# Kernel tuning notes

Hardware: AMD Instinct MI355X
Metric: run time of the kernel (lower is better)

Reference implementation:

```python
import jax, jax.numpy as jnp
import numpy as np

NUM_HEADS = 4
NUM_GROUPS = 32
EPS = 1e-5

def setup_inputs() -> dict:
    key = jax.random.key(0)
    ks = jax.random.split(key, 3)
    B, C, H, W = 16, 512, 32, 32
    x = jax.random.normal(ks[0], (B, C, H, W), dtype=jnp.float32)
    gn_w = jnp.ones((C,), jnp.float32)
    gn_b = jnp.zeros((C,), jnp.float32)
    qkv_w = jax.random.normal(ks[1], (3 * C, C), dtype=jnp.float32) * (C ** -0.5)
    qkv_b = jnp.zeros((3 * C,), jnp.float32)
    proj_w = jax.random.normal(ks[2], (C, C), dtype=jnp.float32) * (C ** -0.5)
    proj_b = jnp.zeros((C,), jnp.float32)
    return {"x": x, "gn_w": gn_w, "gn_b": gn_b, "qkv_w": qkv_w,
            "qkv_b": qkv_b, "proj_w": proj_w, "proj_b": proj_b}

def group_norm(x, w, b):
    B, C, H, W = x.shape
    xg = x.reshape(B, NUM_GROUPS, C // NUM_GROUPS, H, W)
    mean = xg.mean(axis=(2, 3, 4), keepdims=True)
    var = xg.var(axis=(2, 3, 4), keepdims=True)
    xg = (xg - mean) * jax.lax.rsqrt(var + EPS)
    x = xg.reshape(B, C, H, W)
    return x * w[None, :, None, None] + b[None, :, None, None]

def reference(x, gn_w, gn_b, qkv_w, qkv_b, proj_w, proj_b):
    B, C, H, W = x.shape
    hd = C // NUM_HEADS
    h = group_norm(x, gn_w, gn_b)
    # 1x1 conv == channel matmul
    qkv = jnp.einsum('oc,bchw->bohw', qkv_w, h) + qkv_b[None, :, None, None]
    q, k, v = jnp.split(qkv, 3, axis=1)
    N = H * W
    q = q.reshape(B, NUM_HEADS, hd, N)
    k = k.reshape(B, NUM_HEADS, hd, N)
    v = v.reshape(B, NUM_HEADS, hd, N)
    scale = hd ** -0.5
    attn = jnp.einsum('bhcn,bhcm->bhnm', q, k) * scale
    attn = jax.nn.softmax(attn, axis=-1)
    o = jnp.einsum('bhnm,bhcm->bhcn', attn, v).reshape(B, C, H, W)
    o = jnp.einsum('oc,bchw->bohw', proj_w, o) + proj_b[None, :, None, None]
    return x + o
```

## Files before the change

kernel.cpp:

```cpp
#include <hip/hip_runtime.h>

typedef __attribute__((ext_vector_type(4))) float f32x4;
typedef __attribute__((ext_vector_type(8))) short s16x8;

#define MFMA16(a, b, c) __builtin_amdgcn_mfma_f32_16x16x32_bf16((a), (b), (c), 0, 0, 0)

__device__ __forceinline__ unsigned short f2bf(float f) {
    union { float f; unsigned u; } v; v.f = f;
    unsigned u = v.u + 0x7FFFu + ((v.u >> 16) & 1u);
    return (unsigned short)(u >> 16);
}

__device__ __forceinline__ unsigned cvtpk(float lo, float hi) {
    unsigned r;
    asm("v_cvt_pk_bf16_f32 %0, %1, %2" : "=v"(r) : "v"(lo), "v"(hi));
    return r;
}

__device__ __forceinline__ float exp2f_fast(float x) {
    float r;
    asm("v_exp_f32 %0, %1" : "=v"(r) : "v"(x));
    return r;
}

__device__ __forceinline__ void gll16(const unsigned short* g, unsigned short* l) {
    __builtin_amdgcn_global_load_lds((const __attribute__((address_space(1))) void*)g,
                                     (__attribute__((address_space(3))) void*)l, 16, 0, 0);
}

__global__ __launch_bounds__(256) void k_wconv(const float* __restrict__ qkv_w,
                                               const float* __restrict__ proj_w,
                                               unsigned short* __restrict__ wout) {
    int i = blockIdx.x * 256 + threadIdx.x;
    const int NQ = 3 * 512 * 512;
    float v = (i < NQ) ? qkv_w[i] : proj_w[i - NQ];
    wout[i] = f2bf(v);
}

__global__ __launch_bounds__(256) void k_gnstats(const float* __restrict__ x,
                                                 float* __restrict__ stats) {
    int bg = blockIdx.x;
    const float4* p = (const float4*)(x + (size_t)bg * 16384);
    float s = 0.f, ss = 0.f;
    for (int i = threadIdx.x; i < 4096; i += 256) {
        float4 v = p[i];
        s += v.x + v.y + v.z + v.w;
        ss += v.x * v.x + v.y * v.y + v.z * v.z + v.w * v.w;
    }
    for (int w = 1; w < 64; w <<= 1) { s += __shfl_xor(s, w); ss += __shfl_xor(ss, w); }
    __shared__ float rs[4], rss[4];
    int wid = threadIdx.x >> 6;
    if ((threadIdx.x & 63) == 0) { rs[wid] = s; rss[wid] = ss; }
    __syncthreads();
    if (threadIdx.x == 0) {
        float S = rs[0] + rs[1] + rs[2] + rs[3];
        float SS = rss[0] + rss[1] + rss[2] + rss[3];
        float mean = S * (1.f / 16384.f);
        float var = SS * (1.f / 16384.f) - mean * mean;
        stats[bg * 2] = mean;
        stats[bg * 2 + 1] = rsqrtf(var + 1e-5f);
    }
}

__global__ __launch_bounds__(256) void k_gnapply(const float* __restrict__ x,
                                                 const float* __restrict__ gnw,
                                                 const float* __restrict__ gnb,
                                                 const float* __restrict__ stats,
                                                 unsigned short* __restrict__ h_t) {
    int b = blockIdx.x >> 5, nb = blockIdx.x & 31;
    int n0 = nb * 32;
    __shared__ unsigned short lds[32][520];
    int t = threadIdx.x;
    int f4 = t & 7, c0 = t >> 3;
    for (int c = c0; c < 512; c += 32) {
        int g = c >> 4;
        float mean = stats[(b * 32 + g) * 2], rstd = stats[(b * 32 + g) * 2 + 1];
        float sc = gnw[c] * rstd;
        float sh = gnb[c] - mean * sc;
        float4 v = *(const float4*)(x + ((size_t)(b * 512 + c)) * 1024 + n0 + f4 * 4);
        lds[f4 * 4 + 0][c] = f2bf(v.x * sc + sh);
        lds[f4 * 4 + 1][c] = f2bf(v.y * sc + sh);
        lds[f4 * 4 + 2][c] = f2bf(v.z * sc + sh);
        lds[f4 * 4 + 3][c] = f2bf(v.w * sc + sh);
    }
    __syncthreads();
    int ch = t & 63;
    for (int nl = t >> 6; nl < 32; nl += 4) {
        *(uint4*)(h_t + ((size_t)(b * 1024 + n0 + nl)) * 512 + ch * 8) =
            *(const uint4*)(&lds[nl][ch * 8]);
    }
}

__global__ __launch_bounds__(256) void k_gemm(const unsigned short* __restrict__ A,
                                              const unsigned short* __restrict__ Bt,
                                              const float* __restrict__ bias, int mode,
                                              unsigned short* __restrict__ Qo,
                                              unsigned short* __restrict__ Ko,
                                              unsigned short* __restrict__ Vo,
                                              const float* __restrict__ xres,
                                              float* __restrict__ out) {
    const int Kd = 512;
    int id = blockIdx.x;
    int xcd = id & 7, j = id >> 3;
    int nt = xcd + 8 * (j & 15);
    int mt = j >> 4;
    int t = threadIdx.x, wid = t >> 6, lane = t & 63;
    int lm = lane & 15, q4 = lane >> 4;
    int wm = wid >> 1, wn = wid & 1;
    __shared__ unsigned short ldsA[2][4096];
    __shared__ unsigned short ldsB[2][4096];
    int m0 = mt * 128, n0 = nt * 128;

    const unsigned short* gA[2];
    const unsigned short* gB[2];
    unsigned short* dA[2][2];
    unsigned short* dB[2][2];
#pragma unroll
    for (int h = 0; h < 2; ++h) {
        int cib = h * 256 + wid * 64;
        int ci = cib + lane;
        int r = ci >> 2;
        int cc = (ci & 3) ^ (r & 3);
        gA[h] = A + (size_t)(m0 + r) * Kd + cc * 8;
        gB[h] = Bt + (size_t)(n0 + r) * Kd + cc * 8;
        dA[0][h] = &ldsA[0][cib * 8];
        dA[1][h] = &ldsA[1][cib * 8];
        dB[0][h] = &ldsB[0][cib * 8];
        dB[1][h] = &ldsB[1][cib * 8];
    }

    f32x4 z = {0.f, 0.f, 0.f, 0.f};
    f32x4 acc[4][4];
#pragma unroll
    for (int fi = 0; fi < 4; ++fi)
#pragma unroll
        for (int fj = 0; fj < 4; ++fj) acc[fi][fj] = z;

    gll16(gA[0], dA[0][0]); gll16(gB[0], dB[0][0]);
    gll16(gA[1], dA[0][1]); gll16(gB[1], dB[0][1]);
    gA[0] += 32; gA[1] += 32; gB[0] += 32; gB[1] += 32;

    const int NK = 16;
    for (int ks = 0; ks < NK; ++ks) {
        int cur = ks & 1;
        if (ks + 1 < NK) {
            int nb = cur ^ 1;
            gll16(gA[0], dA[nb][0]); gll16(gB[0], dB[nb][0]);
            gll16(gA[1], dA[nb][1]); gll16(gB[1], dB[nb][1]);
            gA[0] += 32; gA[1] += 32; gB[0] += 32; gB[1] += 32;
            asm volatile("s_waitcnt vmcnt(4)" ::: "memory");
        } else {
            asm volatile("s_waitcnt vmcnt(0)" ::: "memory");
        }
        __builtin_amdgcn_s_barrier();
        asm volatile("" ::: "memory");
        const unsigned short* lA = ldsA[cur];
        const unsigned short* lB = ldsB[cur];
        s16x8 af[4], bg[4];
#pragma unroll
        for (int fi = 0; fi < 4; ++fi) {
            int rA = wm * 64 + fi * 16 + lm;
            af[fi] = *(const s16x8*)&lA[(rA * 4 + (q4 ^ (lm & 3))) * 8];
        }
#pragma unroll
        for (int fj = 0; fj < 4; ++fj) {
            int rB = wn * 64 + fj * 16 + lm;
            bg[fj] = *(const s16x8*)&lB[(rB * 4 + (q4 ^ (lm & 3))) * 8];
        }
#pragma unroll
        for (int fi = 0; fi < 4; ++fi)
#pragma unroll
            for (int fj = 0; fj < 4; ++fj) acc[fi][fj] = MFMA16(af[fi], bg[fj], acc[fi][fj]);
        asm volatile("" ::: "memory");
        __builtin_amdgcn_s_barrier();
    }

    if (mode == 0) {
        int part = mt >> 2;
        int head = mt & 3;
        int b = nt >> 3;
        int bh = b * 4 + head;
        const float qscale = 0.08838834764831845f * 1.4426950408889634f;
#pragma unroll
        for (int fi = 0; fi < 4; ++fi) {
            int ddb = wm * 64 + fi * 16 + 4 * q4;
            float bv[4];
#pragma unroll
            for (int i = 0; i < 4; ++i) bv[i] = bias[mt * 128 + ddb + i];
#pragma unroll
            for (int fj = 0; fj < 4; ++fj) {
                int n = ((nt & 7) << 7) + wn * 64 + fj * 16 + lm;
                f32x4 v = acc[fi][fj];
                if (part == 0) {
                    uint2 pr;
                    pr.x = cvtpk((v[0] + bv[0]) * qscale, (v[1] + bv[1]) * qscale);
                    pr.y = cvtpk((v[2] + bv[2]) * qscale, (v[3] + bv[3]) * qscale);
                    *(uint2*)(Qo + ((size_t)bh * 1024 + n) * 128 + ddb) = pr;
                } else if (part == 1) {
                    uint2 pr;
                    pr.x = cvtpk(v[0] + bv[0], v[1] + bv[1]);
                    pr.y = cvtpk(v[2] + bv[2], v[3] + bv[3]);
                    *(uint2*)(Ko + ((size_t)bh * 1024 + n) * 128 + ddb) = pr;
                } else {
                    int r = (fj & 1) * 16 + lm;
                    int kidx = (lm >> 2) * 8 + (fj & 1) * 4 + (lm & 3);
                    int np = n - r + kidx;
#pragma unroll
                    for (int i = 0; i < 4; ++i)
                        Vo[((size_t)bh * 128 + ddb + i) * 1024 + np] = f2bf(v[i] + bv[i]);
                }
            }
        }
    } else {
        int b = nt >> 3;
#pragma unroll
        for (int fi = 0; fi < 4; ++fi) {
            int ocb = m0 + wm * 64 + fi * 16 + 4 * q4;
            float bv[4];
#pragma unroll
            for (int i = 0; i < 4; ++i) bv[i] = bias[ocb + i];
#pragma unroll
            for (int fj = 0; fj < 4; ++fj) {
                int n = ((nt & 7) << 7) + wn * 64 + fj * 16 + lm;
#pragma unroll
                for (int i = 0; i < 4; ++i) {
                    size_t idx = ((size_t)b * 512 + ocb + i) * 1024 + n;
                    out[idx] = xres[idx] + bv[i] + acc[fi][fj][i];
                }
            }
        }
    }
}

__global__ __launch_bounds__(256, 2) void k_attn(const unsigned short* __restrict__ Q,
                                                 const unsigned short* __restrict__ K,
                                                 const unsigned short* __restrict__ V,
                                                 unsigned short* __restrict__ o_t) {
    int id = blockIdx.y * 8 + blockIdx.x;
    int bh = (id & 7) + ((id >> 6) << 3);
    int qb = (id >> 3) & 7;
    int t = threadIdx.x, wid = t >> 6, lane = t & 63;
    int lm = lane & 15, q4 = lane >> 4;
    __shared__ unsigned short ldsK[2][4096];
    __shared__ unsigned short ldsV[2][4096];
    const unsigned short* Qg = Q + ((size_t)bh * 1024 + qb * 128 + wid * 32) * 128;
    const unsigned short* Kg = K + (size_t)bh * 1024 * 128;
    const unsigned short* Vg = V + (size_t)bh * 128 * 1024;

    s16x8 qf0[4], qf1[4];
#pragma unroll
    for (int dc = 0; dc < 4; ++dc) {
        qf0[dc] = *(const s16x8*)&Qg[lm * 128 + dc * 32 + q4 * 8];
        qf1[dc] = *(const s16x8*)&Qg[(16 + lm) * 128 + dc * 32 + q4 * 8];
    }

    const unsigned short* gk[2];
    const unsigned short* gv[2];
    unsigned short* lkd[2][2];
    unsigned short* lvd[2][2];
#pragma unroll
    for (int h = 0; h < 2; ++h) {
        int cib = h * 256 + wid * 64;
        int ci = cib + lane;
        int mr = ci >> 4, cl = ci & 15;
        gk[h] = Kg + mr * 128 + (cl ^ (mr & 7)) * 8;
        int d = ci >> 2, kc = ci & 3;
        gv[h] = Vg + (size_t)d * 1024 + (kc ^ ((d >> 1) & 3)) * 8;
        lkd[0][h] = &ldsK[0][cib * 8];
        lkd[1][h] = &ldsK[1][cib * 8];
        lvd[0][h] = &ldsV[0][cib * 8];
        lvd[1][h] = &ldsV[1][cib * 8];
    }
    gll16(gk[0], lkd[0][0]); gll16(gk[1], lkd[0][1]);
    gll16(gv[0], lvd[0][0]); gll16(gv[1], lvd[0][1]);
    gk[0] += 4096; gk[1] += 4096; gv[0] += 32; gv[1] += 32;

    f32x4 z = {0.f, 0.f, 0.f, 0.f};
    f32x4 oa[8], ob[8];
#pragma unroll
    for (int i = 0; i < 8; ++i) { oa[i] = z; ob[i] = z; }
    float mra = -1e30f, mrb = -1e30f, lpa = 0.f, lpb = 0.f;

    for (int ms = 0; ms < 32; ++ms) {
        int cur = ms & 1;
        if (ms < 31) {
            int nb = cur ^ 1;
            gll16(gk[0], lkd[nb][0]); gll16(gk[1], lkd[nb][1]);
            gll16(gv[0], lvd[nb][0]); gll16(gv[1], lvd[nb][1]);
            gk[0] += 4096; gk[1] += 4096; gv[0] += 32; gv[1] += 32;
            asm volatile("s_waitcnt vmcnt(4)" ::: "memory");
        } else {
            asm volatile("s_waitcnt vmcnt(0)" ::: "memory");
        }
        __builtin_amdgcn_s_barrier();
        const unsigned short* lK = ldsK[cur];
        const unsigned short* lV = ldsV[cur];

        f32x4 s0a = z, s0b = z, s1a = z, s1b = z;
        __builtin_amdgcn_s_setprio(1);
#pragma unroll
        for (int dc = 0; dc < 4; ++dc) {
            int sw = ((dc * 4 + q4) ^ (lm & 7)) * 8;
            s16x8 k0 = *(const s16x8*)&lK[lm * 128 + sw];
            s16x8 k1 = *(const s16x8*)&lK[(16 + lm) * 128 + sw];
            s0a = MFMA16(k0, qf0[dc], s0a);
            s0b = MFMA16(k0, qf1[dc], s0b);
            s1a = MFMA16(k1, qf0[dc], s1a);
            s1b = MFMA16(k1, qf1[dc], s1b);
        }
        __builtin_amdgcn_s_setprio(0);

        float tma = fmaxf(fmaxf(fmaxf(s0a[0], s0a[1]), fmaxf(s0a[2], s0a[3])),
                          fmaxf(fmaxf(s1a[0], s1a[1]), fmaxf(s1a[2], s1a[3])));
        float tmb = fmaxf(fmaxf(fmaxf(s0b[0], s0b[1]), fmaxf(s0b[2], s0b[3])),
                          fmaxf(fmaxf(s1b[0], s1b[1]), fmaxf(s1b[2], s1b[3])));
        if (!__all(tma <= mra + 8.f && tmb <= mrb + 8.f)) {
            tma = fmaxf(tma, __shfl_xor(tma, 16));
            tma = fmaxf(tma, __shfl_xor(tma, 32));
            tmb = fmaxf(tmb, __shfl_xor(tmb, 16));
            tmb = fmaxf(tmb, __shfl_xor(tmb, 32));
            float mna = fmaxf(mra, tma), mnb = fmaxf(mrb, tmb);
            float ca = exp2f_fast(mra - mna), cb = exp2f_fast(mrb - mnb);
            lpa *= ca; lpb *= cb;
#pragma unroll
            for (int t8 = 0; t8 < 8; ++t8)
#pragma unroll
                for (int i = 0; i < 4; ++i) { oa[t8][i] *= ca; ob[t8][i] *= cb; }
            mra = mna; mrb = mnb;
        }
        float pa[8], pb[8];
#pragma unroll
        for (int i = 0; i < 4; ++i) {
            pa[i]     = exp2f_fast(s0a[i] - mra);
            pa[4 + i] = exp2f_fast(s1a[i] - mra);
            pb[i]     = exp2f_fast(s0b[i] - mrb);
            pb[4 + i] = exp2f_fast(s1b[i] - mrb);
        }
#pragma unroll
        for (int i = 0; i < 8; ++i) { lpa += pa[i]; lpb += pb[i]; }
        union { s16x8 v; unsigned u[4]; } fa, fb;
        fa.u[0] = cvtpk(pa[0], pa[1]); fa.u[1] = cvtpk(pa[2], pa[3]);
        fa.u[2] = cvtpk(pa[4], pa[5]); fa.u[3] = cvtpk(pa[6], pa[7]);
        fb.u[0] = cvtpk(pb[0], pb[1]); fb.u[1] = cvtpk(pb[2], pb[3]);
        fb.u[2] = cvtpk(pb[4], pb[5]); fb.u[3] = cvtpk(pb[6], pb[7]);

        __builtin_amdgcn_s_setprio(1);
#pragma unroll
        for (int t8 = 0; t8 < 8; ++t8) {
            int r = t8 * 16 + lm;
            s16x8 vf = *(const s16x8*)&lV[r * 32 + ((q4 ^ ((lm >> 1) & 3)) * 8)];
            oa[t8] = MFMA16(vf, fa.v, oa[t8]);
            ob[t8] = MFMA16(vf, fb.v, ob[t8]);
        }
        __builtin_amdgcn_s_setprio(0);
        __builtin_amdgcn_s_barrier();
    }

    lpa += __shfl_xor(lpa, 16); lpa += __shfl_xor(lpa, 32);
    lpb += __shfl_xor(lpb, 16); lpb += __shfl_xor(lpb, 32);
    float inva = 1.f / lpa, invb = 1.f / lpb;
    int b = bh >> 2, head = bh & 3;
    size_t rowa = (size_t)b * 1024 + qb * 128 + wid * 32 + lm;
    unsigned short* da = o_t + rowa * 512 + head * 128;
    unsigned short* db = da + (size_t)16 * 512;
#pragma unroll
    for (int t8 = 0; t8 < 8; ++t8) {
        uint2 pr;
        pr.x = cvtpk(oa[t8][0] * inva, oa[t8][1] * inva);
        pr.y = cvtpk(oa[t8][2] * inva, oa[t8][3] * inva);
        *(uint2*)&da[t8 * 16 + q4 * 4] = pr;
        pr.x = cvtpk(ob[t8][0] * invb, ob[t8][1] * invb);
        pr.y = cvtpk(ob[t8][2] * invb, ob[t8][3] * invb);
        *(uint2*)&db[t8 * 16 + q4 * 4] = pr;
    }
}

extern "C" void kernel_launch(void* const* d_in, const int* in_sizes, int n_in,
                              void* d_out, int out_size, void* d_ws, size_t ws_size,
                              hipStream_t stream) {
    const float* x = (const float*)d_in[0];
    const float* gnw = (const float*)d_in[1];
    const float* gnb = (const float*)d_in[2];
    const float* qkvw = (const float*)d_in[3];
    const float* qkvb = (const float*)d_in[4];
    const float* projw = (const float*)d_in[5];
    const float* projb = (const float*)d_in[6];
    float* out = (float*)d_out;
    char* ws = (char*)d_ws;

    unsigned short* wq = (unsigned short*)(ws);
    unsigned short* wp = (unsigned short*)(ws + 1572864);
    float* stats = (float*)(ws + 2097152);
    unsigned short* ht = (unsigned short*)(ws + 2101248);
    unsigned short* Qb = (unsigned short*)(ws + 18878464);
    unsigned short* Kb = (unsigned short*)(ws + 35655680);
    unsigned short* Vb = (unsigned short*)(ws + 52432896);
    unsigned short* ot = ht;

    k_wconv<<<dim3(4096), dim3(256), 0, stream>>>(qkvw, projw, wq);
    k_gnstats<<<dim3(512), dim3(256), 0, stream>>>(x, stats);
    k_gnapply<<<dim3(512), dim3(256), 0, stream>>>(x, gnw, gnb, stats, ht);
    k_gemm<<<dim3(1536), dim3(256), 0, stream>>>(wq, ht, qkvb, 0, Qb, Kb, Vb, nullptr, nullptr);
    k_attn<<<dim3(8, 64), dim3(256), 0, stream>>>(Qb, Kb, Vb, ot);
    k_gemm<<<dim3(512), dim3(256), 0, stream>>>(wp, ot, projb, 1, nullptr, nullptr, nullptr, x, out);
}
```

Measured before the change: 131.4 us.

## Fuse group-norm stats and apply kernels; double attention KV tile size

Merges the group-norm statistics and apply kernels into one kernel per (batch, group). The block reuses its 64KB group slab, likely cache-resident, to normalize, then transposes it through LDS into the token-major bf16 layout. This removes a launch and the stats round trip, but the transposed stores now write only 32-byte segments per row. Separately, the attention kernel loads 64 keys per pipeline stage instead of 32, with a new V swizzle. That halves the loop iterations and barriers at the cost of doubled LDS (64KB per block), which may limit occupancy.

Result: faster. 128.5 us (-2.2%).

```diff
diff --git a/kernel.cpp b/kernel.cpp
--- a/kernel.cpp
+++ b/kernel.cpp
@@ -37,57 +37,55 @@
     wout[i] = f2bf(v);
 }
 
-__global__ __launch_bounds__(256) void k_gnstats(const float* __restrict__ x,
-                                                 float* __restrict__ stats) {
+__global__ __launch_bounds__(256) void k_gn(const float* __restrict__ x,
+                                            const float* __restrict__ gnw,
+                                            const float* __restrict__ gnb,
+                                            unsigned short* __restrict__ h_t) {
     int bg = blockIdx.x;
+    int b = bg >> 5, g = bg & 31;
+    int t = threadIdx.x;
     const float4* p = (const float4*)(x + (size_t)bg * 16384);
     float s = 0.f, ss = 0.f;
-    for (int i = threadIdx.x; i < 4096; i += 256) {
+    for (int i = t; i < 4096; i += 256) {
         float4 v = p[i];
         s += v.x + v.y + v.z + v.w;
         ss += v.x * v.x + v.y * v.y + v.z * v.z + v.w * v.w;
     }
     for (int w = 1; w < 64; w <<= 1) { s += __shfl_xor(s, w); ss += __shfl_xor(ss, w); }
-    __shared__ float rs[4], rss[4];
-    int wid = threadIdx.x >> 6;
-    if ((threadIdx.x & 63) == 0) { rs[wid] = s; rss[wid] = ss; }
+    __shared__ float rs[4], rss[4], mv[2];
+    __shared__ unsigned short ldt[1024][18];
+    int wid = t >> 6;
+    if ((t & 63) == 0) { rs[wid] = s; rss[wid] = ss; }
     __syncthreads();
-    if (threadIdx.x == 0) {
+    if (t == 0) {
         float S = rs[0] + rs[1] + rs[2] + rs[3];
         float SS = rss[0] + rss[1] + rss[2] + rss[3];
         float mean = S * (1.f / 16384.f);
         float var = SS * (1.f / 16384.f) - mean * mean;
-        stats[bg * 2] = mean;
-        stats[bg * 2 + 1] = rsqrtf(var + 1e-5f);
-    }
-}
-
-__global__ __launch_bounds__(256) void k_gnapply(const float* __restrict__ x,
-                                                 const float* __restrict__ gnw,
-                                                 const float* __restrict__ gnb,
-                                                 const float* __restrict__ stats,
-                                                 unsigned short* __restrict__ h_t) {
-    int b = blockIdx.x >> 5, nb = blockIdx.x & 31;
-    int n0 = nb * 32;
-    __shared__ unsigned short lds[32][520];
-    int t = threadIdx.x;
-    int f4 = t & 7, c0 = t >> 3;
-    for (int c = c0; c < 512; c += 32) {
-        int g = c >> 4;
-        float mean = stats[(b * 32 + g) * 2], rstd = stats[(b * 32 + g) * 2 + 1];
-        float sc = gnw[c] * rstd;
-        float sh = gnb[c] - mean * sc;
-        float4 v = *(const float4*)(x + ((size_t)(b * 512 + c)) * 1024 + n0 + f4 * 4);
-        lds[f4 * 4 + 0][c] = f2bf(v.x * sc + sh);
-        lds[f4 * 4 + 1][c] = f2bf(v.y * sc + sh);
-        lds[f4 * 4 + 2][c] = f2bf(v.z * sc + sh);
-        lds[f4 * 4 + 3][c] = f2bf(v.w * sc + sh);
+        mv[0] = mean; mv[1] = rsqrtf(var + 1e-5f);
     }
     __syncthreads();
-    int ch = t & 63;
-    for (int nl = t >> 6; nl < 32; nl += 4) {
-        *(uint4*)(h_t + ((size_t)(b * 1024 + n0 + nl)) * 512 + ch * 8) =
-            *(const uint4*)(&lds[nl][ch * 8]);
+    int c = t >> 4, f4 = t & 15;
+    float mean = mv[0], rstd = mv[1];
+    float sc = gnw[g * 16 + c] * rstd;
+    float sh = gnb[g * 16 + c] - mean * sc;
+    const float4* pc = (const float4*)(x + ((size_t)(b * 512 + g * 16 + c)) * 1024);
+#pragma unroll
+    for (int i = 0; i < 16; ++i) {
+        int n = i * 64 + f4 * 4;
+        float4 v = pc[n >> 2];
+        ldt[n + 0][c] = f2bf(v.x * sc + sh);
+        ldt[n + 1][c] = f2bf(v.y * sc + sh);
+        ldt[n + 2][c] = f2bf(v.z * sc + sh);
+        ldt[n + 3][c] = f2bf(v.w * sc + sh);
+    }
+    __syncthreads();
+    int half = t & 1;
+#pragma unroll
+    for (int i = 0; i < 8; ++i) {
+        int row = i * 128 + (t >> 1);
+        *(uint4*)(h_t + ((size_t)(b * 1024 + row)) * 512 + g * 16 + half * 8) =
+            *(const uint4*)(&ldt[row][half * 8]);
     }
 }
 
@@ -241,8 +239,8 @@
     int qb = (id >> 3) & 7;
     int t = threadIdx.x, wid = t >> 6, lane = t & 63;
     int lm = lane & 15, q4 = lane >> 4;
-    __shared__ unsigned short ldsK[2][4096];
-    __shared__ unsigned short ldsV[2][4096];
+    __shared__ unsigned short ldsK[2][8192];
+    __shared__ unsigned short ldsV[2][8192];
     const unsigned short* Qg = Q + ((size_t)bh * 1024 + qb * 128 + wid * 32) * 128;
     const unsigned short* Kg = K + (size_t)bh * 1024 * 128;
     const unsigned short* Vg = V + (size_t)bh * 128 * 1024;
@@ -254,26 +252,27 @@
         qf1[dc] = *(const s16x8*)&Qg[(16 + lm) * 128 + dc * 32 + q4 * 8];
     }
 
-    const unsigned short* gk[2];
-    const unsigned short* gv[2];
-    unsigned short* lkd[2][2];
-    unsigned short* lvd[2][2];
-#pragma unroll
-    for (int h = 0; h < 2; ++h) {
+    const unsigned short* gk[4];
+    const unsigned short* gv[4];
+    unsigned short* lkd[2][4];
+    unsigned short* lvd[2][4];
+#pragma unroll
+    for (int h = 0; h < 4; ++h) {
         int cib = h * 256 + wid * 64;
         int ci = cib + lane;
         int mr = ci >> 4, cl = ci & 15;
         gk[h] = Kg + mr * 128 + (cl ^ (mr & 7)) * 8;
-        int d = ci >> 2, kc = ci & 3;
-        gv[h] = Vg + (size_t)d * 1024 + (kc ^ ((d >> 1) & 3)) * 8;
+        int d = ci >> 3, kc = ci & 7;
+        gv[h] = Vg + (size_t)d * 1024 + (kc ^ (d & 7)) * 8;
         lkd[0][h] = &ldsK[0][cib * 8];
         lkd[1][h] = &ldsK[1][cib * 8];
         lvd[0][h] = &ldsV[0][cib * 8];
         lvd[1][h] = &ldsV[1][cib * 8];
     }
-    gll16(gk[0], lkd[0][0]); gll16(gk[1], lkd[0][1]);
-    gll16(gv[0], lvd[0][0]); gll16(gv[1], lvd[0][1]);
-    gk[0] += 4096; gk[1] += 4096; gv[0] += 32; gv[1] += 32;
+#pragma unroll
+    for (int h = 0; h < 4; ++h) { gll16(gk[h], lkd[0][h]); gll16(gv[h], lvd[0][h]); }
+#pragma unroll
+    for (int h = 0; h < 4; ++h) { gk[h] += 8192; gv[h] += 64; }
 
     f32x4 z = {0.f, 0.f, 0.f, 0.f};
     f32x4 oa[8], ob[8];
@@ -281,14 +280,15 @@
     for (int i = 0; i < 8; ++i) { oa[i] = z; ob[i] = z; }
     float mra = -1e30f, mrb = -1e30f, lpa = 0.f, lpb = 0.f;
 
-    for (int ms = 0; ms < 32; ++ms) {
+    for (int ms = 0; ms < 16; ++ms) {
         int cur = ms & 1;
-        if (ms < 31) {
+        if (ms < 15) {
             int nb = cur ^ 1;
-            gll16(gk[0], lkd[nb][0]); gll16(gk[1], lkd[nb][1]);
-            gll16(gv[0], lvd[nb][0]); gll16(gv[1], lvd[nb][1]);
-            gk[0] += 4096; gk[1] += 4096; gv[0] += 32; gv[1] += 32;
-            asm volatile("s_waitcnt vmcnt(4)" ::: "memory");
+#pragma unroll
+            for (int h = 0; h < 4; ++h) { gll16(gk[h], lkd[nb][h]); gll16(gv[h], lvd[nb][h]); }
+#pragma unroll
+            for (int h = 0; h < 4; ++h) { gk[h] += 8192; gv[h] += 64; }
+            asm volatile("s_waitcnt vmcnt(8)" ::: "memory");
         } else {
             asm volatile("s_waitcnt vmcnt(0)" ::: "memory");
         }
@@ -296,63 +296,66 @@
         const unsigned short* lK = ldsK[cur];
         const unsigned short* lV = ldsV[cur];
 
-        f32x4 s0a = z, s0b = z, s1a = z, s1b = z;
-        __builtin_amdgcn_s_setprio(1);
-#pragma unroll
-        for (int dc = 0; dc < 4; ++dc) {
-            int sw = ((dc * 4 + q4) ^ (lm & 7)) * 8;
-            s16x8 k0 = *(const s16x8*)&lK[lm * 128 + sw];
-            s16x8 k1 = *(const s16x8*)&lK[(16 + lm) * 128 + sw];
-            s0a = MFMA16(k0, qf0[dc], s0a);
-            s0b = MFMA16(k0, qf1[dc], s0b);
-            s1a = MFMA16(k1, qf0[dc], s1a);
-            s1b = MFMA16(k1, qf1[dc], s1b);
-        }
-        __builtin_amdgcn_s_setprio(0);
-
-        float tma = fmaxf(fmaxf(fmaxf(s0a[0], s0a[1]), fmaxf(s0a[2], s0a[3])),
-                          fmaxf(fmaxf(s1a[0], s1a[1]), fmaxf(s1a[2], s1a[3])));
-        float tmb = fmaxf(fmaxf(fmaxf(s0b[0], s0b[1]), fmaxf(s0b[2], s0b[3])),
-                          fmaxf(fmaxf(s1b[0], s1b[1]), fmaxf(s1b[2], s1b[3])));
-        if (!__all(tma <= mra + 8.f && tmb <= mrb + 8.f)) {
-            tma = fmaxf(tma, __shfl_xor(tma, 16));
-            tma = fmaxf(tma, __shfl_xor(tma, 32));
-            tmb = fmaxf(tmb, __shfl_xor(tmb, 16));
-            tmb = fmaxf(tmb, __shfl_xor(tmb, 32));
-            float mna = fmaxf(mra, tma), mnb = fmaxf(mrb, tmb);
-            float ca = exp2f_fast(mra - mna), cb = exp2f_fast(mrb - mnb);
-            lpa *= ca; lpb *= cb;
-#pragma unroll
-            for (int t8 = 0; t8 < 8; ++t8)
-#pragma unroll
-                for (int i = 0; i < 4; ++i) { oa[t8][i] *= ca; ob[t8][i] *= cb; }
-            mra = mna; mrb = mnb;
-        }
-        float pa[8], pb[8];
-#pragma unroll
-        for (int i = 0; i < 4; ++i) {
-            pa[i]     = exp2f_fast(s0a[i] - mra);
-            pa[4 + i] = exp2f_fast(s1a[i] - mra);
-            pb[i]     = exp2f_fast(s0b[i] - mrb);
-            pb[4 + i] = exp2f_fast(s1b[i] - mrb);
-        }
-#pragma unroll
-        for (int i = 0; i < 8; ++i) { lpa += pa[i]; lpb += pb[i]; }
-        union { s16x8 v; unsigned u[4]; } fa, fb;
-        fa.u[0] = cvtpk(pa[0], pa[1]); fa.u[1] = cvtpk(pa[2], pa[3]);
-        fa.u[2] = cvtpk(pa[4], pa[5]); fa.u[3] = cvtpk(pa[6], pa[7]);
-        fb.u[0] = cvtpk(pb[0], pb[1]); fb.u[1] = cvtpk(pb[2], pb[3]);
-        fb.u[2] = cvtpk(pb[4], pb[5]); fb.u[3] = cvtpk(pb[6], pb[7]);
-
-        __builtin_amdgcn_s_setprio(1);
-#pragma unroll
-        for (int t8 = 0; t8 < 8; ++t8) {
-            int r = t8 * 16 + lm;
-            s16x8 vf = *(const s16x8*)&lV[r * 32 + ((q4 ^ ((lm >> 1) & 3)) * 8)];
-            oa[t8] = MFMA16(vf, fa.v, oa[t8]);
-            ob[t8] = MFMA16(vf, fb.v, ob[t8]);
-        }
-        __builtin_amdgcn_s_setprio(0);
+#pragma unroll
+        for (int hk = 0; hk < 2; ++hk) {
+            f32x4 s0a = z, s0b = z, s1a = z, s1b = z;
+            __builtin_amdgcn_s_setprio(1);
+#pragma unroll
+            for (int dc = 0; dc < 4; ++dc) {
+                int sw = ((dc * 4 + q4) ^ (lm & 7)) * 8;
+                s16x8 k0 = *(const s16x8*)&lK[(hk * 32 + lm) * 128 + sw];
+                s16x8 k1 = *(const s16x8*)&lK[(hk * 32 + 16 + lm) * 128 + sw];
+                s0a = MFMA16(k0, qf0[dc], s0a);
+                s0b = MFMA16(k0, qf1[dc], s0b);
+                s1a = MFMA16(k1, qf0[dc], s1a);
+                s1b = MFMA16(k1, qf1[dc], s1b);
+            }
+            __builtin_amdgcn_s_setprio(0);
+
+            float tma = fmaxf(fmaxf(fmaxf(s0a[0], s0a[1]), fmaxf(s0a[2], s0a[3])),
+                              fmaxf(fmaxf(s1a[0], s1a[1]), fmaxf(s1a[2], s1a[3])));
+            float tmb = fmaxf(fmaxf(fmaxf(s0b[0], s0b[1]), fmaxf(s0b[2], s0b[3])),
+                              fmaxf(fmaxf(s1b[0], s1b[1]), fmaxf(s1b[2], s1b[3])));
+            if (!__all(tma <= mra + 8.f && tmb <= mrb + 8.f)) {
+                tma = fmaxf(tma, __shfl_xor(tma, 16));
+                tma = fmaxf(tma, __shfl_xor(tma, 32));
+                tmb = fmaxf(tmb, __shfl_xor(tmb, 16));
+                tmb = fmaxf(tmb, __shfl_xor(tmb, 32));
+                float mna = fmaxf(mra, tma), mnb = fmaxf(mrb, tmb);
+                float ca = exp2f_fast(mra - mna), cb = exp2f_fast(mrb - mnb);
+                lpa *= ca; lpb *= cb;
+#pragma unroll
+                for (int t8 = 0; t8 < 8; ++t8)
+#pragma unroll
+                    for (int i = 0; i < 4; ++i) { oa[t8][i] *= ca; ob[t8][i] *= cb; }
+                mra = mna; mrb = mnb;
+            }
+            float pa[8], pb[8];
+#pragma unroll
+            for (int i = 0; i < 4; ++i) {
+                pa[i]     = exp2f_fast(s0a[i] - mra);
+                pa[4 + i] = exp2f_fast(s1a[i] - mra);
+                pb[i]     = exp2f_fast(s0b[i] - mrb);
+                pb[4 + i] = exp2f_fast(s1b[i] - mrb);
+            }
+#pragma unroll
+            for (int i = 0; i < 8; ++i) { lpa += pa[i]; lpb += pb[i]; }
+            union { s16x8 v; unsigned u[4]; } fa, fb;
+            fa.u[0] = cvtpk(pa[0], pa[1]); fa.u[1] = cvtpk(pa[2], pa[3]);
+            fa.u[2] = cvtpk(pa[4], pa[5]); fa.u[3] = cvtpk(pa[6], pa[7]);
+            fb.u[0] = cvtpk(pb[0], pb[1]); fb.u[1] = cvtpk(pb[2], pb[3]);
+            fb.u[2] = cvtpk(pb[4], pb[5]); fb.u[3] = cvtpk(pb[6], pb[7]);
+
+            __builtin_amdgcn_s_setprio(1);
+#pragma unroll
+            for (int t8 = 0; t8 < 8; ++t8) {
+                int r = t8 * 16 + lm;
+                s16x8 vf = *(const s16x8*)&lV[r * 64 + (((hk * 4 + q4) ^ (lm & 7)) * 8)];
+                oa[t8] = MFMA16(vf, fa.v, oa[t8]);
+                ob[t8] = MFMA16(vf, fb.v, ob[t8]);
+            }
+            __builtin_amdgcn_s_setprio(0);
+        }
         __builtin_amdgcn_s_barrier();
     }
 
@@ -390,7 +393,6 @@
 
     unsigned short* wq = (unsigned short*)(ws);
     unsigned short* wp = (unsigned short*)(ws + 1572864);
-    float* stats = (float*)(ws + 2097152);
     unsigned short* ht = (unsigned short*)(ws + 2101248);
     unsigned short* Qb = (unsigned short*)(ws + 18878464);
     unsigned short* Kb = (unsigned short*)(ws + 35655680);
@@ -398,8 +400,7 @@
     unsigned short* ot = ht;
 
     k_wconv<<<dim3(4096), dim3(256), 0, stream>>>(qkvw, projw, wq);
-    k_gnstats<<<dim3(512), dim3(256), 0, stream>>>(x, stats);
-    k_gnapply<<<dim3(512), dim3(256), 0, stream>>>(x, gnw, gnb, stats, ht);
+    k_gn<<<dim3(512), dim3(256), 0, stream>>>(x, gnw, gnb, ht);
     k_gemm<<<dim3(1536), dim3(256), 0, stream>>>(wq, ht, qkvb, 0, Qb, Kb, Vb, nullptr, nullptr);
     k_attn<<<dim3(8, 64), dim3(256), 0, stream>>>(Qb, Kb, Vb, ot);
     k_gemm<<<dim3(512), dim3(256), 0, stream>>>(wp, ot, projb, 1, nullptr, nullptr, nullptr, x, out);
```
